# Kernel optimization log

Hardware: AMD Instinct MI355X
Metric: run time of the kernel (lower is better)

The kernel has to match this reference:

```python
import jax, jax.numpy as jnp
import numpy as np

B, T, E = 2, 2048, 2048
H, HKV, M = 16, 4, 4
HD = E // H // M          # 32
NREP = H // HKV           # 4
EPS = 1e-5


def _rotary_interleaved(x, cos, sin):
    # x: (B, S, nh, HD); cos/sin: (S, HD//2), interleaved pairs (0::2, 1::2)
    x1 = x[..., 0::2]
    x2 = x[..., 1::2]
    c = cos[None, :, None, :]
    s = sin[None, :, None, :]
    o1 = x1 * c - x2 * s
    o2 = x1 * s + x2 * c
    return jnp.stack([o1, o2], axis=-1).reshape(x.shape)


def setup_inputs() -> dict:
    key = jax.random.key(0)
    ks = jax.random.split(key, 6)
    x = jax.random.normal(ks[0], (B, T, E), jnp.float32)
    pos = jnp.arange(T, dtype=jnp.float32)
    inv_freq = 1.0 / (10000.0 ** (jnp.arange(0, HD, 2, dtype=jnp.float32) / HD))
    ang = pos[:, None] * inv_freq[None, :]  # (T, HD//2)
    cos = jnp.cos(ang)
    sin = jnp.sin(ang)
    s = 0.02
    q_w = jax.random.normal(ks[1], (E, E), jnp.float32) * s
    k_w = jax.random.normal(ks[2], (E // NREP, E), jnp.float32) * s
    v_w = jax.random.normal(ks[3], (E // NREP, E), jnp.float32) * s
    out_w = jax.random.normal(ks[4], (E, E), jnp.float32) * s
    raw_map_weights = jnp.array([0.1 * (-1.0) ** i for i in range(M)], jnp.float32)
    weight_scale = jnp.ones((1,), jnp.float32)
    gamma = jnp.ones((M * HD,), jnp.float32)
    return dict(x=x, cos=cos, sin=sin, q_w=q_w, k_w=k_w, v_w=v_w, out_w=out_w,
                raw_map_weights=raw_map_weights, weight_scale=weight_scale, gamma=gamma)


def reference(x, cos, sin, q_w, k_w, v_w, out_w, raw_map_weights, weight_scale, gamma):
    # projections
    q = (x @ q_w.T).reshape(B, T, M * H, HD)
    k = (x @ k_w.T).reshape(B, T, M * HKV, HD)
    v = (x @ v_w.T).reshape(B, T, HKV, M * HD)
    # rotary (interleaved) on full head_dim, then split heads x maps (heads major, maps minor)
    q = _rotary_interleaved(q, cos, sin).reshape(B, T, H, M, HD)
    k = _rotary_interleaved(k, cos, sin).reshape(B, T, HKV, M, HD)
    # GQA: q head h attends to kv head h // NREP  (repeat_interleave semantics)
    k_rep = jnp.repeat(k, NREP, axis=2)  # (B,T,H,M,HD)
    v_rep = jnp.repeat(v, NREP, axis=2)  # (B,T,H,M*HD)
    map_w = jnp.tanh(raw_map_weights) * weight_scale[0]
    scale = HD ** -0.5  # flash_attn default softmax scale
    causal = jnp.tril(jnp.ones((T, T), dtype=bool))
    combined = jnp.zeros((B, T, H, M * HD), x.dtype)
    for i in range(M):  # small fixed num_maps loop
        scores = jnp.einsum('bqhd,bkhd->bhqk', q[:, :, :, i], k_rep[:, :, :, i]) * scale
        scores = jnp.where(causal[None, None], scores, -jnp.inf)
        p = jax.nn.softmax(scores, axis=-1)
        attn_i = jnp.einsum('bhqk,bkhe->bqhe', p, v_rep)  # (B,T,H,M*HD)
        combined = combined + map_w[i] * attn_i
    # RMSNorm over last dim (num_maps * head_dim) with affine weight
    var = jnp.mean(combined * combined, axis=-1, keepdims=True)
    normed = combined * jax.lax.rsqrt(var + EPS) * gamma
    out = normed.reshape(B, T, E) @ out_w.T
    return out
```

## Files before the change

kernel.cpp:

```cpp
#include <hip/hip_runtime.h>


typedef unsigned short u16;
typedef unsigned int u32;
typedef _Float16 f16;
typedef _Float16 f16x8 __attribute__((ext_vector_type(8)));
typedef float f32x4 __attribute__((ext_vector_type(4)));

#define B_ 2
#define T_ 2048
#define E_ 2048
#define H_ 16
#define HKV_ 4
#define M_ 4
#define HD_ 32
#define SCALE_Q 0.2550348873f

#define GLOAD_LDS(g, l)                                                   \
  __builtin_amdgcn_global_load_lds(                                       \
      (const __attribute__((address_space(1))) u32*)(g),                  \
      (__attribute__((address_space(3))) u32*)(l), 16, 0, 0)

__device__ __forceinline__ u16 f2h(float f) {
  f16 h = (f16)f;
  return __builtin_bit_cast(u16, h);
}

__global__ void cvt_all(const float* __restrict__ x, const float* __restrict__ qw,
                        const float* __restrict__ kw, const float* __restrict__ vw,
                        const float* __restrict__ ow, u16* __restrict__ xb,
                        u16* __restrict__ wcat, u16* __restrict__ wo16) {
  const float* src;
  u16* dst;
  int n4;
  switch (blockIdx.y) {
    case 0: src = x;  dst = xb;            n4 = 2097152; break;
    case 1: src = qw; dst = wcat;          n4 = 1048576; break;
    case 2: src = kw; dst = wcat + 4194304; n4 = 262144; break;
    case 3: src = vw; dst = wcat + 5242880; n4 = 262144; break;
    default: src = ow; dst = wo16;         n4 = 1048576; break;
  }
  int i = blockIdx.x * blockDim.x + threadIdx.x;
  if (i < n4) {
    float4 v = ((const float4*)src)[i];
    ushort4 o;
    o.x = f2h(v.x); o.y = f2h(v.y); o.z = f2h(v.z); o.w = f2h(v.w);
    ((ushort4*)dst)[i] = o;
  }
}

__global__ __launch_bounds__(256) void gemm_bt(const u16* __restrict__ A,
                                               const u16* __restrict__ Bm,
                                               float* __restrict__ C,
                                               int M, int N, int K) {
  __shared__ __align__(16) u16 As[128 * 32];
  __shared__ __align__(16) u16 Bs[128 * 32];
  const int tid = threadIdx.x;
  const int lane = tid & 63;
  const int wv = tid >> 6;
  const int g = lane >> 4;
  const int r = lane & 15;
  const int m0 = blockIdx.y * 128;
  const int n0 = blockIdx.x * 128;
  const int wm = (wv >> 1) * 64;
  const int wn = (wv & 1) * 64;

  f32x4 acc[4][4];
#pragma unroll
  for (int a = 0; a < 4; ++a)
#pragma unroll
    for (int b = 0; b < 4; ++b) acc[a][b] = (f32x4){0.f, 0.f, 0.f, 0.f};

  const int r0 = tid >> 2;
  const int c8 = (tid & 3) << 3;

  for (int k0 = 0; k0 < K; k0 += 32) {
#pragma unroll
    for (int j = 0; j < 2; ++j) {
      GLOAD_LDS(&A[(size_t)(m0 + r0 + j * 64) * K + k0 + c8], &As[tid * 8 + j * 2048]);
      GLOAD_LDS(&Bm[(size_t)(n0 + r0 + j * 64) * K + k0 + c8], &Bs[tid * 8 + j * 2048]);
    }
    __syncthreads();
    f16x8 af[4], bfr[4];
#pragma unroll
    for (int mt = 0; mt < 4; ++mt)
      af[mt] = *(const f16x8*)&As[(wm + mt * 16 + r) * 32 + g * 8];
#pragma unroll
    for (int nt = 0; nt < 4; ++nt)
      bfr[nt] = *(const f16x8*)&Bs[(wn + nt * 16 + r) * 32 + g * 8];
#pragma unroll
    for (int mt = 0; mt < 4; ++mt)
#pragma unroll
      for (int nt = 0; nt < 4; ++nt)
        acc[mt][nt] = __builtin_amdgcn_mfma_f32_16x16x32_f16(af[mt], bfr[nt], acc[mt][nt], 0, 0, 0);
    __syncthreads();
  }
#pragma unroll
  for (int mt = 0; mt < 4; ++mt)
#pragma unroll
    for (int nt = 0; nt < 4; ++nt) {
      int row = m0 + wm + mt * 16 + g * 4;
      int col = n0 + wn + nt * 16 + r;
#pragma unroll
      for (int rr = 0; rr < 4; ++rr)
        C[(size_t)(row + rr) * N + col] = acc[mt][nt][rr];
    }
}

__global__ void rope_repack(const float* __restrict__ qkv,
                            const float* __restrict__ cosb,
                            const float* __restrict__ sinb,
                            u16* __restrict__ qp, u16* __restrict__ kp,
                            u16* __restrict__ vtp) {
  int gid = blockIdx.x * blockDim.x + threadIdx.x;
  int rt = gid / 1536;
  int cp = (gid - rt * 1536) * 2;
  int b = rt >> 11;
  int t = rt & 2047;
  const float* src = qkv + (size_t)rt * 3072 + cp;
  float x1 = src[0], x2 = src[1];
  if (cp < 2048) {
    int hh = cp >> 7, mm = (cp >> 5) & 3, d = cp & 31;
    int j = d >> 1;
    float c = cosb[t * 16 + j], s = sinb[t * 16 + j];
    size_t dst = ((((size_t)b * H_ + hh) * M_ + mm) * T_ + t) * HD_ + d;
    qp[dst] = f2h((x1 * c - x2 * s) * SCALE_Q);
    qp[dst + 1] = f2h((x1 * s + x2 * c) * SCALE_Q);
  } else if (cp < 2560) {
    int c2 = cp - 2048;
    int hh = c2 >> 7, mm = (c2 >> 5) & 3, d = c2 & 31;
    int j = d >> 1;
    float c = cosb[t * 16 + j], s = sinb[t * 16 + j];
    size_t dst = ((((size_t)b * HKV_ + hh) * M_ + mm) * T_ + t) * HD_ + d;
    kp[dst] = f2h(x1 * c - x2 * s);
    kp[dst + 1] = f2h(x1 * s + x2 * c);
  } else {
    int c2 = cp - 2560;
    int hh = c2 >> 7, e = c2 & 127;
    size_t base = ((size_t)b * HKV_ + hh) * 128;
    vtp[(base + e) * T_ + t] = f2h(x1);
    vtp[(base + e + 1) * T_ + t] = f2h(x2);
  }
}

__global__ __launch_bounds__(256) void lstats_kernel(
    const u16* __restrict__ qp, const u16* __restrict__ kp,
    const float* __restrict__ rawW, const float* __restrict__ wscale,
    float* __restrict__ invw) {
  const int tid = threadIdx.x;
  const int lane = tid & 63;
  const int wv = tid >> 6;
  const int g = lane >> 4, r = lane & 15;
  const int h = blockIdx.y;
  const int b = blockIdx.z >> 2, e = blockIdx.z & 3;
  const int hkv = h >> 2;
  const int s0 = blockIdx.x * 4 + wv;

  const size_t qb = (((size_t)b * H_ + h) * M_ + e) * T_ * HD_;
  const size_t kb = (((size_t)b * HKV_ + hkv) * M_ + e) * T_ * HD_;
  const float mw = tanhf(rawW[e]) * wscale[0];

  for (int ps = 0; ps < 2; ++ps) {
    const int strip = ps ? 127 - s0 : s0;
    const int q0 = strip * 16;
    f16x8 qf = *(const f16x8*)&qp[qb + (size_t)(q0 + r) * HD_ + g * 8];
    float lacc[4] = {0.f, 0.f, 0.f, 0.f};

    for (int k0 = 0; k0 < q0 + 16; k0 += 64) {
      f32x4 s[4];
#pragma unroll
      for (int nt = 0; nt < 4; ++nt) {
        f16x8 kf = *(const f16x8*)&kp[kb + (size_t)(k0 + nt * 16 + r) * HD_ + g * 8];
        s[nt] = __builtin_amdgcn_mfma_f32_16x16x32_f16(qf, kf, (f32x4){0.f, 0.f, 0.f, 0.f}, 0, 0, 0);
      }
#pragma unroll
      for (int rr = 0; rr < 4; ++rr) {
        int row = q0 + g * 4 + rr;
#pragma unroll
        for (int nt = 0; nt < 4; ++nt) {
          int col = k0 + nt * 16 + r;
          float ev = exp2f(s[nt][rr]);
          lacc[rr] += (col <= row) ? ev : 0.f;
        }
      }
    }
#pragma unroll
    for (int rr = 0; rr < 4; ++rr) {
      float l = lacc[rr];
#pragma unroll
      for (int off = 8; off >= 1; off >>= 1) l += __shfl_xor(l, off, 64);
      if (r == 0)
        invw[(((size_t)b * H_ + h) * M_ + e) * T_ + q0 + g * 4 + rr] = mw / l;
    }
  }
}

__global__ __launch_bounds__(256) void attn_kernel(
    const u16* __restrict__ qp, const u16* __restrict__ kp,
    const u16* __restrict__ vtp, const float* __restrict__ invw,
    const float* __restrict__ gamma, u16* __restrict__ normed) {
  __shared__ __align__(16) char smem[64 * 132 * 4];
  u16* Ks = (u16*)smem;
  u16* Pc = (u16*)(smem + 16384);
  float* comb = (float*)smem;

  const int tid = threadIdx.x;
  const int lane = tid & 63;
  const int wv = tid >> 6;
  const int g = lane >> 4;
  const int r = lane & 15;
  const int h = blockIdx.y;
  const int b = blockIdx.z;
  const int hkv = h >> 2;

  const size_t qb = ((size_t)b * H_ + h) * M_ * T_ * HD_;
  const size_t kb = ((size_t)b * HKV_ + hkv) * M_ * T_ * HD_;
  const size_t vb = ((size_t)b * HKV_ + hkv) * 128 * (size_t)T_;

#define STAGE_KS(K0)                                                          \
  {                                                                           \
    _Pragma("unroll") for (int j = 0; j < 4; ++j) {                           \
      int f = tid + j * 256;                                                  \
      int e_ = f >> 8, g2 = (f >> 6) & 3, kk = f & 63;                        \
      GLOAD_LDS(&kp[kb + ((size_t)e_ * T_ + (K0) + kk) * HD_ + g2 * 8],       \
                &Ks[f * 8]);                                                  \
    }                                                                         \
  }

  for (int ps = 0; ps < 2; ++ps) {
    const int q0 = (ps ? 31 - blockIdx.x : blockIdx.x) * 64;
    const int rq = q0 + wv * 16;

    f16x8 qf[4];
    float iw[4][4];
#pragma unroll
    for (int e = 0; e < 4; ++e) {
      qf[e] = *(const f16x8*)&qp[qb + ((size_t)e * T_ + rq + r) * HD_ + g * 8];
      const float* ivp = invw + (((size_t)b * H_ + h) * M_ + e) * T_;
#pragma unroll
      for (int rr = 0; rr < 4; ++rr) iw[e][rr] = ivp[rq + g * 4 + rr];
    }

    f32x4 acc[4][2];
#pragma unroll
    for (int mt = 0; mt < 4; ++mt)
#pragma unroll
      for (int v2 = 0; v2 < 2; ++v2) acc[mt][v2] = (f32x4){0.f, 0.f, 0.f, 0.f};

    __syncthreads();
    STAGE_KS(0);
    __syncthreads();

    const int nk = q0 + 64;
    for (int k0 = 0; k0 < nk; k0 += 64) {
      float pc[4][4];
      if (k0 <= rq + 15) {
        const bool need_mask = (k0 + 63 > rq);
#pragma unroll
        for (int e = 0; e < 4; ++e) {
          f32x4 s[4];
#pragma unroll
          for (int nt = 0; nt < 4; ++nt) {
            f16x8 kf = *(const f16x8*)&Ks[e * 2048 + g * 512 + (nt * 16 + r) * 8];
            s[nt] = __builtin_amdgcn_mfma_f32_16x16x32_f16(qf[e], kf, (f32x4){0.f, 0.f, 0.f, 0.f}, 0, 0, 0);
          }
#pragma unroll
          for (int nt = 0; nt < 4; ++nt)
#pragma unroll
            for (int rr = 0; rr < 4; ++rr) {
              float p = exp2f(s[nt][rr]) * iw[e][rr];
              if (need_mask && (k0 + nt * 16 + r > rq + g * 4 + rr)) p = 0.f;
              pc[nt][rr] = (e == 0) ? p : pc[nt][rr] + p;
            }
        }
      } else {
#pragma unroll
        for (int nt = 0; nt < 4; ++nt)
#pragma unroll
          for (int rr = 0; rr < 4; ++rr) pc[nt][rr] = 0.f;
      }

      f16x8 vf[2][2];
#pragma unroll
      for (int v2 = 0; v2 < 2; ++v2)
#pragma unroll
        for (int k2 = 0; k2 < 2; ++k2)
          vf[v2][k2] = *(const f16x8*)&vtp[vb + (size_t)(wv * 32 + v2 * 16 + r) * T_ + k0 + k2 * 32 + g * 8];

      __syncthreads();

#pragma unroll
      for (int nt = 0; nt < 4; ++nt)
#pragma unroll
        for (int rr = 0; rr < 4; ++rr)
          Pc[(wv * 16 + g * 4 + rr) * 72 + nt * 16 + r] = f2h(pc[nt][rr]);

      if (k0 + 64 < nk) STAGE_KS(k0 + 64);

      __syncthreads();

#pragma unroll
      for (int mt = 0; mt < 4; ++mt) {
        f16x8 pf0 = *(const f16x8*)&Pc[(mt * 16 + r) * 72 + g * 8];
        f16x8 pf1 = *(const f16x8*)&Pc[(mt * 16 + r) * 72 + 32 + g * 8];
#pragma unroll
        for (int v2 = 0; v2 < 2; ++v2) {
          acc[mt][v2] = __builtin_amdgcn_mfma_f32_16x16x32_f16(pf0, vf[v2][0], acc[mt][v2], 0, 0, 0);
          acc[mt][v2] = __builtin_amdgcn_mfma_f32_16x16x32_f16(pf1, vf[v2][1], acc[mt][v2], 0, 0, 0);
        }
      }
    }

    __syncthreads();
#pragma unroll
    for (int mt = 0; mt < 4; ++mt)
#pragma unroll
      for (int v2 = 0; v2 < 2; ++v2)
#pragma unroll
        for (int rr = 0; rr < 4; ++rr)
          comb[(mt * 16 + g * 4 + rr) * 132 + wv * 32 + v2 * 16 + r] = acc[mt][v2][rr];
    __syncthreads();

    {
      int row = tid >> 2;
      int ch = (tid & 3) * 32;
      float vals[32];
      float ss = 0.f;
#pragma unroll
      for (int e2 = 0; e2 < 32; ++e2) {
        float v = comb[row * 132 + ch + e2];
        vals[e2] = v;
        ss += v * v;
      }
      ss += __shfl_xor(ss, 1, 64);
      ss += __shfl_xor(ss, 2, 64);
      float rstd = rsqrtf(ss * (1.f / 128.f) + 1e-5f);
      size_t obase = ((size_t)b * T_ + q0 + row) * E_ + (size_t)h * 128 + ch;
      union { u16 u[32]; uint4 q[4]; } pk;
#pragma unroll
      for (int e2 = 0; e2 < 32; ++e2)
        pk.u[e2] = f2h(vals[e2] * rstd * gamma[ch + e2]);
#pragma unroll
      for (int qq = 0; qq < 4; ++qq)
        *(uint4*)&normed[obase + qq * 8] = pk.q[qq];
    }
  }
#undef STAGE_KS
}

extern "C" void kernel_launch(void* const* d_in, const int* in_sizes, int n_in,
                              void* d_out, int out_size, void* d_ws, size_t ws_size,
                              hipStream_t stream) {
  const float* x = (const float*)d_in[0];
  const float* cosb = (const float*)d_in[1];
  const float* sinb = (const float*)d_in[2];
  const float* qw = (const float*)d_in[3];
  const float* kw = (const float*)d_in[4];
  const float* vw = (const float*)d_in[5];
  const float* ow = (const float*)d_in[6];
  const float* rawW = (const float*)d_in[7];
  const float* wsc = (const float*)d_in[8];
  const float* gm = (const float*)d_in[9];
  float* out = (float*)d_out;

  char* ws = (char*)d_ws;
  u16* xb = (u16*)(ws);
  u16* wcat = (u16*)(ws + (16ull << 20));
  u16* wo16 = (u16*)(ws + (28ull << 20));
  float* qkv = (float*)(ws + (36ull << 20));
  float* invw = (float*)(ws + (36ull << 20));
  u16* qp = (u16*)(ws + (84ull << 20));
  u16* kp = (u16*)(ws + (100ull << 20));
  u16* vtp = (u16*)(ws + (104ull << 20));
  u16* normed = xb;

  cvt_all<<<dim3(8192, 5), 256, 0, stream>>>(x, qw, kw, vw, ow, xb, wcat, wo16);
  gemm_bt<<<dim3(3072 / 128, 4096 / 128), 256, 0, stream>>>(xb, wcat, qkv, 4096, 3072, 2048);
  rope_repack<<<(4096 * 1536) / 256, 256, 0, stream>>>(qkv, cosb, sinb, qp, kp, vtp);
  lstats_kernel<<<dim3(16, H_, B_ * M_), 256, 0, stream>>>(qp, kp, rawW, wsc, invw);
  attn_kernel<<<dim3(16, H_, B_), 256, 0, stream>>>(qp, kp, vtp, invw, gm, normed);
  gemm_bt<<<dim3(2048 / 128, 4096 / 128), 256, 0, stream>>>(normed, wo16, out, 4096, 2048, 2048);
}
```

Baseline: 501.6 us.

## Fuse rotary and repack into QKV GEMM epilogue; double-buffer K tiles in attention

The QKV projection GEMM now applies interleaved rotary and the Q scale in its epilogue, using a lane shuffle to fetch the pair element. It writes fp16 Q/K/V directly in attention layout, which removes the fp32 qkv round trip and the separate rope_repack launch. The attention kernel double-buffers K staging in LDS so the next tile's load is issued before the current compute, and hoists the V fragment loads earlier. Masking now sets the score to -1e30 before exp2 and accumulates with fma, at the cost of more LDS per block and a more complex epilogue.

```diff
diff --git a/kernel.cpp b/kernel.cpp
--- a/kernel.cpp
+++ b/kernel.cpp
@@ -48,6 +48,27 @@
     ((ushort4*)dst)[i] = o;
   }
 }
+
+#define GEMM_CORE(A_, B_ptr, K_)                                              \
+  for (int k0 = 0; k0 < (K_); k0 += 32) {                                     \
+    _Pragma("unroll") for (int j = 0; j < 2; ++j) {                           \
+      GLOAD_LDS(&(A_)[(size_t)(m0 + r0 + j * 64) * (K_) + k0 + c8],           \
+                &As[tid * 8 + j * 2048]);                                     \
+      GLOAD_LDS(&(B_ptr)[(size_t)(n0 + r0 + j * 64) * (K_) + k0 + c8],        \
+                &Bs[tid * 8 + j * 2048]);                                     \
+    }                                                                         \
+    __syncthreads();                                                          \
+    f16x8 af[4], bfr[4];                                                      \
+    _Pragma("unroll") for (int mt = 0; mt < 4; ++mt)                          \
+        af[mt] = *(const f16x8*)&As[(wm + mt * 16 + r) * 32 + g * 8];         \
+    _Pragma("unroll") for (int nt = 0; nt < 4; ++nt)                          \
+        bfr[nt] = *(const f16x8*)&Bs[(wn + nt * 16 + r) * 32 + g * 8];        \
+    _Pragma("unroll") for (int mt = 0; mt < 4; ++mt)                          \
+        _Pragma("unroll") for (int nt = 0; nt < 4; ++nt)                      \
+            acc[mt][nt] = __builtin_amdgcn_mfma_f32_16x16x32_f16(             \
+                af[mt], bfr[nt], acc[mt][nt], 0, 0, 0);                       \
+    __syncthreads();                                                          \
+  }
 
 __global__ __launch_bounds__(256) void gemm_bt(const u16* __restrict__ A,
                                                const u16* __restrict__ Bm,
@@ -64,37 +85,16 @@
   const int n0 = blockIdx.x * 128;
   const int wm = (wv >> 1) * 64;
   const int wn = (wv & 1) * 64;
-
   f32x4 acc[4][4];
 #pragma unroll
   for (int a = 0; a < 4; ++a)
 #pragma unroll
     for (int b = 0; b < 4; ++b) acc[a][b] = (f32x4){0.f, 0.f, 0.f, 0.f};
-
   const int r0 = tid >> 2;
   const int c8 = (tid & 3) << 3;
 
-  for (int k0 = 0; k0 < K; k0 += 32) {
-#pragma unroll
-    for (int j = 0; j < 2; ++j) {
-      GLOAD_LDS(&A[(size_t)(m0 + r0 + j * 64) * K + k0 + c8], &As[tid * 8 + j * 2048]);
-      GLOAD_LDS(&Bm[(size_t)(n0 + r0 + j * 64) * K + k0 + c8], &Bs[tid * 8 + j * 2048]);
-    }
-    __syncthreads();
-    f16x8 af[4], bfr[4];
-#pragma unroll
-    for (int mt = 0; mt < 4; ++mt)
-      af[mt] = *(const f16x8*)&As[(wm + mt * 16 + r) * 32 + g * 8];
-#pragma unroll
-    for (int nt = 0; nt < 4; ++nt)
-      bfr[nt] = *(const f16x8*)&Bs[(wn + nt * 16 + r) * 32 + g * 8];
-#pragma unroll
-    for (int mt = 0; mt < 4; ++mt)
-#pragma unroll
-      for (int nt = 0; nt < 4; ++nt)
-        acc[mt][nt] = __builtin_amdgcn_mfma_f32_16x16x32_f16(af[mt], bfr[nt], acc[mt][nt], 0, 0, 0);
-    __syncthreads();
-  }
+  GEMM_CORE(A, Bm, K)
+
 #pragma unroll
   for (int mt = 0; mt < 4; ++mt)
 #pragma unroll
@@ -107,39 +107,98 @@
     }
 }
 
-__global__ void rope_repack(const float* __restrict__ qkv,
-                            const float* __restrict__ cosb,
-                            const float* __restrict__ sinb,
-                            u16* __restrict__ qp, u16* __restrict__ kp,
-                            u16* __restrict__ vtp) {
-  int gid = blockIdx.x * blockDim.x + threadIdx.x;
-  int rt = gid / 1536;
-  int cp = (gid - rt * 1536) * 2;
-  int b = rt >> 11;
-  int t = rt & 2047;
-  const float* src = qkv + (size_t)rt * 3072 + cp;
-  float x1 = src[0], x2 = src[1];
-  if (cp < 2048) {
-    int hh = cp >> 7, mm = (cp >> 5) & 3, d = cp & 31;
-    int j = d >> 1;
-    float c = cosb[t * 16 + j], s = sinb[t * 16 + j];
-    size_t dst = ((((size_t)b * H_ + hh) * M_ + mm) * T_ + t) * HD_ + d;
-    qp[dst] = f2h((x1 * c - x2 * s) * SCALE_Q);
-    qp[dst + 1] = f2h((x1 * s + x2 * c) * SCALE_Q);
-  } else if (cp < 2560) {
-    int c2 = cp - 2048;
-    int hh = c2 >> 7, mm = (c2 >> 5) & 3, d = c2 & 31;
-    int j = d >> 1;
-    float c = cosb[t * 16 + j], s = sinb[t * 16 + j];
-    size_t dst = ((((size_t)b * HKV_ + hh) * M_ + mm) * T_ + t) * HD_ + d;
-    kp[dst] = f2h(x1 * c - x2 * s);
-    kp[dst + 1] = f2h(x1 * s + x2 * c);
+__global__ __launch_bounds__(256) void gemm_qkv_rope(
+    const u16* __restrict__ A, const u16* __restrict__ Bm,
+    const float* __restrict__ cosb, const float* __restrict__ sinb,
+    u16* __restrict__ qp, u16* __restrict__ kp, u16* __restrict__ vtp) {
+  __shared__ __align__(16) u16 As[128 * 32];
+  __shared__ __align__(16) u16 Bs[128 * 32];
+  const int tid = threadIdx.x;
+  const int lane = tid & 63;
+  const int wv = tid >> 6;
+  const int g = lane >> 4;
+  const int r = lane & 15;
+  const int m0 = blockIdx.y * 128;
+  const int n0 = blockIdx.x * 128;
+  const int wm = (wv >> 1) * 64;
+  const int wn = (wv & 1) * 64;
+  f32x4 acc[4][4];
+#pragma unroll
+  for (int a = 0; a < 4; ++a)
+#pragma unroll
+    for (int b = 0; b < 4; ++b) acc[a][b] = (f32x4){0.f, 0.f, 0.f, 0.f};
+  const int r0 = tid >> 2;
+  const int c8 = (tid & 3) << 3;
+
+  GEMM_CORE(A, Bm, 2048)
+
+  const int b = m0 >> 11;
+  const float signf = (r & 1) ? 1.f : -1.f;
+  const int jb = r >> 1;
+
+  if (n0 < 2048) {
+#pragma unroll
+    for (int mt = 0; mt < 4; ++mt) {
+      int row = m0 + wm + mt * 16 + g * 4;
+      int t0 = row & 2047;
+#pragma unroll
+      for (int rr = 0; rr < 4; ++rr) {
+        int t = t0 + rr;
+        float c0 = cosb[t * 16 + jb], s0 = sinb[t * 16 + jb];
+        float c1 = cosb[t * 16 + 8 + jb], s1 = sinb[t * 16 + 8 + jb];
+#pragma unroll
+        for (int nt = 0; nt < 4; ++nt) {
+          float xv = acc[mt][nt][rr];
+          float pv = __shfl_xor(xv, 1, 64);
+          float c = (nt & 1) ? c1 : c0;
+          float s = (nt & 1) ? s1 : s0;
+          float o = (xv * c + signf * pv * s) * SCALE_Q;
+          int col = n0 + wn + nt * 16 + r;
+          int hh = col >> 7, mm = (col >> 5) & 3, d = col & 31;
+          qp[((((size_t)b * H_ + hh) * M_ + mm) * T_ + t) * HD_ + d] = f2h(o);
+        }
+      }
+    }
+  } else if (n0 < 2560) {
+#pragma unroll
+    for (int mt = 0; mt < 4; ++mt) {
+      int row = m0 + wm + mt * 16 + g * 4;
+      int t0 = row & 2047;
+#pragma unroll
+      for (int rr = 0; rr < 4; ++rr) {
+        int t = t0 + rr;
+        float c0 = cosb[t * 16 + jb], s0 = sinb[t * 16 + jb];
+        float c1 = cosb[t * 16 + 8 + jb], s1 = sinb[t * 16 + 8 + jb];
+#pragma unroll
+        for (int nt = 0; nt < 4; ++nt) {
+          float xv = acc[mt][nt][rr];
+          float pv = __shfl_xor(xv, 1, 64);
+          float c = (nt & 1) ? c1 : c0;
+          float s = (nt & 1) ? s1 : s0;
+          float o = xv * c + signf * pv * s;
+          int col2 = n0 + wn + nt * 16 + r - 2048;
+          int hh = col2 >> 7, mm = (col2 >> 5) & 3, d = col2 & 31;
+          kp[((((size_t)b * HKV_ + hh) * M_ + mm) * T_ + t) * HD_ + d] = f2h(o);
+        }
+      }
+    }
   } else {
-    int c2 = cp - 2560;
-    int hh = c2 >> 7, e = c2 & 127;
-    size_t base = ((size_t)b * HKV_ + hh) * 128;
-    vtp[(base + e) * T_ + t] = f2h(x1);
-    vtp[(base + e + 1) * T_ + t] = f2h(x2);
+#pragma unroll
+    for (int mt = 0; mt < 4; ++mt) {
+      int row = m0 + wm + mt * 16 + g * 4;
+      int t0 = row & 2047;
+#pragma unroll
+      for (int nt = 0; nt < 4; ++nt) {
+        int col3 = n0 + wn + nt * 16 + r - 2560;
+        int hkv = col3 >> 7, e = col3 & 127;
+        ushort4 w;
+        w.x = f2h(acc[mt][nt][0]);
+        w.y = f2h(acc[mt][nt][1]);
+        w.z = f2h(acc[mt][nt][2]);
+        w.w = f2h(acc[mt][nt][3]);
+        *(ushort4*)&vtp[(((size_t)b * HKV_ + hkv) * 128 + e) * T_ + t0] = w;
+      }
+    }
   }
 }
 
@@ -179,8 +238,8 @@
 #pragma unroll
         for (int nt = 0; nt < 4; ++nt) {
           int col = k0 + nt * 16 + r;
-          float ev = exp2f(s[nt][rr]);
-          lacc[rr] += (col <= row) ? ev : 0.f;
+          float sv = (col <= row) ? s[nt][rr] : -1e30f;
+          lacc[rr] += exp2f(sv);
         }
       }
     }
@@ -199,9 +258,9 @@
     const u16* __restrict__ qp, const u16* __restrict__ kp,
     const u16* __restrict__ vtp, const float* __restrict__ invw,
     const float* __restrict__ gamma, u16* __restrict__ normed) {
-  __shared__ __align__(16) char smem[64 * 132 * 4];
+  __shared__ __align__(16) char smem[42240];
   u16* Ks = (u16*)smem;
-  u16* Pc = (u16*)(smem + 16384);
+  u16* Pc = (u16*)(smem + 32768);
   float* comb = (float*)smem;
 
   const int tid = threadIdx.x;
@@ -217,13 +276,13 @@
   const size_t kb = ((size_t)b * HKV_ + hkv) * M_ * T_ * HD_;
   const size_t vb = ((size_t)b * HKV_ + hkv) * 128 * (size_t)T_;
 
-#define STAGE_KS(K0)                                                          \
+#define STAGE_KS(K0, DST)                                                     \
   {                                                                           \
     _Pragma("unroll") for (int j = 0; j < 4; ++j) {                           \
       int f = tid + j * 256;                                                  \
       int e_ = f >> 8, g2 = (f >> 6) & 3, kk = f & 63;                        \
       GLOAD_LDS(&kp[kb + ((size_t)e_ * T_ + (K0) + kk) * HD_ + g2 * 8],       \
-                &Ks[f * 8]);                                                  \
+                &(DST)[f * 8]);                                               \
     }                                                                         \
   }
 
@@ -248,12 +307,29 @@
       for (int v2 = 0; v2 < 2; ++v2) acc[mt][v2] = (f32x4){0.f, 0.f, 0.f, 0.f};
 
     __syncthreads();
-    STAGE_KS(0);
+    STAGE_KS(0, (u16*)smem);
     __syncthreads();
 
-    const int nk = q0 + 64;
-    for (int k0 = 0; k0 < nk; k0 += 64) {
+    const int niter = q0 / 64 + 1;
+    for (int i = 0; i < niter; ++i) {
+      const int k0 = i * 64;
+      u16* kbuf = (u16*)smem + (size_t)(i & 1) * 8192;
+      u16* knext = (u16*)smem + (size_t)((i + 1) & 1) * 8192;
+
+      if (i + 1 < niter) STAGE_KS(k0 + 64, knext);
+
+      f16x8 vf[2][2];
+#pragma unroll
+      for (int v2 = 0; v2 < 2; ++v2)
+#pragma unroll
+        for (int k2 = 0; k2 < 2; ++k2)
+          vf[v2][k2] = *(const f16x8*)&vtp[vb + (size_t)(wv * 32 + v2 * 16 + r) * T_ + k0 + k2 * 32 + g * 8];
+
       float pc[4][4];
+#pragma unroll
+      for (int nt = 0; nt < 4; ++nt)
+#pragma unroll
+        for (int rr = 0; rr < 4; ++rr) pc[nt][rr] = 0.f;
       if (k0 <= rq + 15) {
         const bool need_mask = (k0 + 63 > rq);
 #pragma unroll
@@ -261,31 +337,19 @@
           f32x4 s[4];
 #pragma unroll
           for (int nt = 0; nt < 4; ++nt) {
-            f16x8 kf = *(const f16x8*)&Ks[e * 2048 + g * 512 + (nt * 16 + r) * 8];
+            f16x8 kf = *(const f16x8*)&kbuf[e * 2048 + g * 512 + (nt * 16 + r) * 8];
             s[nt] = __builtin_amdgcn_mfma_f32_16x16x32_f16(qf[e], kf, (f32x4){0.f, 0.f, 0.f, 0.f}, 0, 0, 0);
           }
 #pragma unroll
           for (int nt = 0; nt < 4; ++nt)
 #pragma unroll
             for (int rr = 0; rr < 4; ++rr) {
-              float p = exp2f(s[nt][rr]) * iw[e][rr];
-              if (need_mask && (k0 + nt * 16 + r > rq + g * 4 + rr)) p = 0.f;
-              pc[nt][rr] = (e == 0) ? p : pc[nt][rr] + p;
+              float sv = s[nt][rr];
+              if (need_mask && (k0 + nt * 16 + r > rq + g * 4 + rr)) sv = -1e30f;
+              pc[nt][rr] = fmaf(exp2f(sv), iw[e][rr], pc[nt][rr]);
             }
         }
-      } else {
-#pragma unroll
-        for (int nt = 0; nt < 4; ++nt)
-#pragma unroll
-          for (int rr = 0; rr < 4; ++rr) pc[nt][rr] = 0.f;
-      }
-
-      f16x8 vf[2][2];
-#pragma unroll
-      for (int v2 = 0; v2 < 2; ++v2)
-#pragma unroll
-        for (int k2 = 0; k2 < 2; ++k2)
-          vf[v2][k2] = *(const f16x8*)&vtp[vb + (size_t)(wv * 32 + v2 * 16 + r) * T_ + k0 + k2 * 32 + g * 8];
+      }
 
       __syncthreads();
 
@@ -294,8 +358,6 @@
 #pragma unroll
         for (int rr = 0; rr < 4; ++rr)
           Pc[(wv * 16 + g * 4 + rr) * 72 + nt * 16 + r] = f2h(pc[nt][rr]);
-
-      if (k0 + 64 < nk) STAGE_KS(k0 + 64);
 
       __syncthreads();
 
@@ -367,7 +429,6 @@
   u16* xb = (u16*)(ws);
   u16* wcat = (u16*)(ws + (16ull << 20));
   u16* wo16 = (u16*)(ws + (28ull << 20));
-  float* qkv = (float*)(ws + (36ull << 20));
   float* invw = (float*)(ws + (36ull << 20));
   u16* qp = (u16*)(ws + (84ull << 20));
   u16* kp = (u16*)(ws + (100ull << 20));
@@ -375,8 +436,7 @@
   u16* normed = xb;
 
   cvt_all<<<dim3(8192, 5), 256, 0, stream>>>(x, qw, kw, vw, ow, xb, wcat, wo16);
-  gemm_bt<<<dim3(3072 / 128, 4096 / 128), 256, 0, stream>>>(xb, wcat, qkv, 4096, 3072, 2048);
-  rope_repack<<<(4096 * 1536) / 256, 256, 0, stream>>>(qkv, cosb, sinb, qp, kp, vtp);
+  gemm_qkv_rope<<<dim3(24, 32), 256, 0, stream>>>(xb, wcat, cosb, sinb, qp, kp, vtp);
   lstats_kernel<<<dim3(16, H_, B_ * M_), 256, 0, stream>>>(qp, kp, rawW, wsc, invw);
   attn_kernel<<<dim3(16, H_, B_), 256, 0, stream>>>(qp, kp, vtp, invw, gm, normed);
   gemm_bt<<<dim3(2048 / 128, 4096 / 128), 256, 0, stream>>>(normed, wo16, out, 4096, 2048, 2048);
```

Measured after the change: 481.9 us. 3.9% less time.
